# Performance work log

Measured on AMD Instinct MI355X. Metric: run time of the kernel, lower is better.

The kernel has to match this reference:

```python
import jax, jax.numpy as jnp
import numpy as np

N_NODES = 10000
N_EDGES = 160000
N_GRAPHS = 64
D_IN = 128
D_H = 512
N_CLS = 2
L = 3
EPS = 1e-7   # GENConv message eps / clamp min
MAXV = 10.0  # GENConv power-mean clamp max
BN_EPS = 1e-5


def setup_inputs() -> dict:
    key = jax.random.key(0)
    ks = jax.random.split(key, 8)
    return {
        "x": jax.random.normal(ks[0], (N_NODES, D_IN), jnp.float32),
        "W0": jax.random.normal(ks[1], (D_IN, D_H), jnp.float32) * 0.05,
        "Wrest": jax.random.normal(ks[2], (L - 1, D_H, D_H), jnp.float32) * 0.05,
        "bconv": jnp.zeros((L, D_H), jnp.float32),
        "p": jnp.ones((L,), jnp.float32),
        "msg_scale": jnp.ones((L,), jnp.float32),
        "bn_gamma": jnp.ones((L, D_H), jnp.float32),
        "bn_beta": jnp.zeros((L, D_H), jnp.float32),
        "fc1_W": jax.random.normal(ks[3], (2 * D_H, D_H), jnp.float32) * 0.05,
        "fc1_b": jnp.zeros((D_H,), jnp.float32),
        "bn4_g": jnp.ones((D_H,), jnp.float32),
        "bn4_b": jnp.zeros((D_H,), jnp.float32),
        "fc2_W": jax.random.normal(ks[4], (D_H, N_CLS), jnp.float32) * 0.05,
        "fc2_b": jnp.zeros((N_CLS,), jnp.float32),
        "edge_index": jax.random.randint(ks[5], (2, N_EDGES), 0, N_NODES, dtype=jnp.int32),
        "batch": jnp.sort(jax.random.randint(ks[6], (N_NODES,), 0, N_GRAPHS, dtype=jnp.int32)),
    }


def _batchnorm(h, g, b):
    # training-mode BatchNorm1d: batch statistics, biased variance
    mu = h.mean(axis=0)
    var = ((h - mu) ** 2).mean(axis=0)
    return (h - mu) * jax.lax.rsqrt(var + BN_EPS) * g + b


def _genconv(x, W, b, p, scale, src, dst):
    # message: m_e = relu(x_src) + eps  (no edge_attr), clamped to [eps, 10]
    m = jnp.minimum(jax.nn.relu(x[src]) + EPS, MAXV)          # [E, d]
    # power-mean aggregation onto target nodes
    deg = jax.ops.segment_sum(jnp.ones((src.shape[0],), x.dtype), dst, N_NODES)
    agg = jax.ops.segment_sum(m ** p, dst, N_NODES) / jnp.maximum(deg, 1.0)[:, None]
    agg = jnp.clip(agg, EPS, MAXV) ** (1.0 / p)               # [N, d]
    # MessageNorm: l2-normalize aggregated message, rescale by ||x|| * scale
    msg = agg / jnp.maximum(jnp.linalg.norm(agg, axis=-1, keepdims=True), 1e-12)
    xn = jnp.linalg.norm(x, axis=-1, keepdims=True)
    out = x + msg * xn * scale                                # residual add
    return out @ W + b                                        # 1-layer MLP


def reference(x, W0, Wrest, bconv, p, msg_scale, bn_gamma, bn_beta,
              fc1_W, fc1_b, bn4_g, bn4_b, fc2_W, fc2_b, edge_index, batch):
    src, dst = edge_index[0], edge_index[1]
    h = x
    jk = None
    for i in range(L):
        W = W0 if i == 0 else Wrest[i - 1]
        h = _genconv(h, W, bconv[i], p[i], msg_scale[i], src, dst)
        h = jax.nn.relu(_batchnorm(h, bn_gamma[i], bn_beta[i]))
        jk = h if jk is None else jnp.maximum(jk, h)          # JumpingKnowledge 'max'
    # global max + mean pooling per graph
    cnt = jax.ops.segment_sum(jnp.ones((N_NODES,), h.dtype), batch, N_GRAPHS)
    gmean = jax.ops.segment_sum(jk, batch, N_GRAPHS) / jnp.maximum(cnt, 1.0)[:, None]
    gmax = jax.ops.segment_max(jk, batch, N_GRAPHS)
    gmax = jnp.where(cnt[:, None] > 0, gmax, 0.0)
    g = jnp.concatenate([gmax, gmean], axis=1)                # [G, 1024]
    g = jax.nn.relu(_batchnorm(g @ fc1_W + fc1_b, bn4_g, bn4_b))
    # dropout: eval mode (identity)
    return g @ fc2_W + fc2_b                                  # [G, num_classes]
```

## Files before the change

kernel.cpp:

```cpp
#include <hip/hip_runtime.h>
#include <hip/hip_bf16.h>
#include <math.h>

#define N_NODES 10000
#define N_GRAPHS 64
#define N_EDGES 160000
#define D_INPUT 128
#define D_H 512
#define EPS 1e-7f
#define MAXV 10.0f
#define BN_EPS 1e-5f
#define M_PAD 10112

typedef __attribute__((ext_vector_type(4))) float f32x4;
typedef __attribute__((ext_vector_type(8))) __bf16 bf16x8;

__global__ __launch_bounds__(256) void hist_kernel(const int* __restrict__ dst,
                                                   int* __restrict__ cnt) {
  int i = blockIdx.x * blockDim.x + threadIdx.x;
  if (i < N_EDGES) atomicAdd(&cnt[dst[i]], 1);
}

__global__ __launch_bounds__(256) void scan_kernel(int* __restrict__ cnt,
                                                   int* __restrict__ rowptr) {
  __shared__ int ps[256];
  int tid = threadIdx.x;
  const int CH = 40;
  int b0 = tid * CH;
  bool active = (b0 < N_NODES);
  int v[CH];
  int s = 0;
  if (active) {
    const int4* c4p = (const int4*)(cnt + b0);
#pragma unroll
    for (int i = 0; i < CH / 4; i++) {
      int4 q = c4p[i];
      v[4 * i] = q.x; v[4 * i + 1] = q.y; v[4 * i + 2] = q.z; v[4 * i + 3] = q.w;
      s += q.x + q.y + q.z + q.w;
    }
  }
  ps[tid] = s;
  __syncthreads();
  for (int off = 1; off < 256; off <<= 1) {
    int t = (tid >= off) ? ps[tid - off] : 0;
    __syncthreads();
    ps[tid] += t;
    __syncthreads();
  }
  int run = (tid == 0) ? 0 : ps[tid - 1];
  if (active) {
    int r[CH];
#pragma unroll
    for (int i = 0; i < CH; i++) { r[i] = run; run += v[i]; }
    int4* rp = (int4*)(rowptr + b0);
    int4* cz = (int4*)(cnt + b0);
#pragma unroll
    for (int i = 0; i < CH / 4; i++) {
      rp[i] = make_int4(r[4 * i], r[4 * i + 1], r[4 * i + 2], r[4 * i + 3]);
      cz[i] = make_int4(0, 0, 0, 0);
    }
  }
  if (tid == 255) rowptr[N_NODES] = ps[255];
}

__global__ __launch_bounds__(256) void scatter_kernel(
    const int* __restrict__ src, const int* __restrict__ dst,
    const int* __restrict__ rowptr, int* __restrict__ cursor,
    int* __restrict__ csr_src) {
  int i = blockIdx.x * blockDim.x + threadIdx.x;
  if (i < N_EDGES) {
    int t = dst[i];
    int pos = rowptr[t] + atomicAdd(&cursor[t], 1);
    csr_src[pos] = src[i];
  }
}

__global__ __launch_bounds__(512) void bn_affine(float* __restrict__ stats,
                                                 const float* __restrict__ gamma,
                                                 const float* __restrict__ beta,
                                                 float* __restrict__ aff) {
  int c = threadIdx.x;
  const float invN = 1.0f / (float)N_NODES;
  float mean = stats[c] * invN;
  float var = stats[D_H + c] * invN - mean * mean;
  float sc = rsqrtf(var + BN_EPS) * gamma[c];
  aff[c] = sc;
  aff[D_H + c] = beta[c] - mean * sc;
  stats[c] = 0.f;
  stats[D_H + c] = 0.f;
}

__global__ __launch_bounds__(256) void msg0_kernel(const float* __restrict__ x,
                                                   const float* __restrict__ p_ptr,
                                                   __hip_bfloat16* __restrict__ msgb) {
  float p = *p_ptr;
  bool p1 = (p == 1.0f);
  const int total = N_NODES * D_INPUT / 2;
  for (int i = blockIdx.x * 256 + threadIdx.x; i < total; i += gridDim.x * 256) {
    float2 v = ((const float2*)x)[i];
    float m0 = fminf(fmaxf(v.x, 0.f) + EPS, MAXV);
    float m1 = fminf(fmaxf(v.y, 0.f) + EPS, MAXV);
    if (!p1) { m0 = powf(m0, p); m1 = powf(m1, p); }
    __hip_bfloat162 o;
    o.x = __float2bfloat16(m0);
    o.y = __float2bfloat16(m1);
    ((__hip_bfloat162*)msgb)[i] = o;
  }
}

template <int D, bool BN>
__global__ __launch_bounds__(256) void agg_msgnorm_kernel(
    const float* __restrict__ h, const float* __restrict__ aff,
    const __hip_bfloat16* __restrict__ msgb,
    const int* __restrict__ rowptr, const int* __restrict__ csr_src,
    const float* __restrict__ p_ptr, const float* __restrict__ scale_ptr,
    __hip_bfloat16* __restrict__ out) {
  constexpr int C = D / 2;
  constexpr int SL = 256 / C;
  int n = blockIdx.x;
  int tid = threadIdx.x;
  int col = tid % C;
  int slice = tid / C;
  int lo = rowptr[n], hi = rowptr[n + 1];
  float p = *p_ptr;
  float scale = *scale_ptr;
  bool p1 = (p == 1.0f);
  float invp = 1.0f / p;
  float inv_dg = 1.0f / fmaxf((float)(hi - lo), 1.0f);
  const float2* h2 = (const float2*)h;
  const uint* mg = (const uint*)msgb;

  __shared__ int s_src[256];
  float accx = 0.f, accy = 0.f;
  for (int base = lo; base < hi; base += 256) {
    int m = min(256, hi - base);
    __syncthreads();
    if (tid < m) s_src[tid] = csr_src[base + tid];
    __syncthreads();
    int j = slice;
    for (; j + 3 * SL < m; j += 4 * SL) {
      uint u0 = mg[(size_t)s_src[j] * C + col];
      uint u1 = mg[(size_t)s_src[j + SL] * C + col];
      uint u2 = mg[(size_t)s_src[j + 2 * SL] * C + col];
      uint u3 = mg[(size_t)s_src[j + 3 * SL] * C + col];
      accx += (__uint_as_float(u0 << 16) + __uint_as_float(u1 << 16)) +
              (__uint_as_float(u2 << 16) + __uint_as_float(u3 << 16));
      accy += (__uint_as_float(u0 & 0xFFFF0000u) + __uint_as_float(u1 & 0xFFFF0000u)) +
              (__uint_as_float(u2 & 0xFFFF0000u) + __uint_as_float(u3 & 0xFFFF0000u));
    }
    for (; j < m; j += SL) {
      uint u = mg[(size_t)s_src[j] * C + col];
      accx += __uint_as_float(u << 16);
      accy += __uint_as_float(u & 0xFFFF0000u);
    }
  }

  if constexpr (SL > 1) {
    __shared__ float sacc[2][256];
    sacc[0][tid] = accx;
    sacc[1][tid] = accy;
    __syncthreads();
    if (tid < C) {
#pragma unroll
      for (int s = 1; s < SL; s++) {
        accx += sacc[0][s * C + tid];
        accy += sacc[1][s * C + tid];
      }
    }
  }

  float a0 = 0.f, a1 = 0.f, hv0 = 0.f, hv1 = 0.f, sa = 0.f, sh = 0.f;
  if (tid < C) {
    a0 = fminf(fmaxf(accx * inv_dg, EPS), MAXV);
    a1 = fminf(fmaxf(accy * inv_dg, EPS), MAXV);
    if (!p1) { a0 = powf(a0, invp); a1 = powf(a1, invp); }
    float2 hx = h2[(size_t)n * C + tid];
    if constexpr (BN) {
      float2 s2 = ((const float2*)aff)[tid];
      float2 b2 = ((const float2*)(aff + D_H))[tid];
      hx.x = fmaxf(hx.x * s2.x + b2.x, 0.f);
      hx.y = fmaxf(hx.y * s2.y + b2.y, 0.f);
    }
    hv0 = hx.x;
    hv1 = hx.y;
    sa = a0 * a0 + a1 * a1;
    sh = hv0 * hv0 + hv1 * hv1;
  }
  for (int off = 32; off; off >>= 1) {
    sa += __shfl_down(sa, off);
    sh += __shfl_down(sh, off);
  }
  __shared__ float red[2][4];
  __shared__ float tot[2];
  int wid = tid >> 6;
  if ((tid & 63) == 0) { red[0][wid] = sa; red[1][wid] = sh; }
  __syncthreads();
  if (tid == 0) {
    tot[0] = red[0][0] + red[0][1] + red[0][2] + red[0][3];
    tot[1] = red[1][0] + red[1][1] + red[1][2] + red[1][3];
  }
  __syncthreads();
  float k = sqrtf(tot[1]) * scale / fmaxf(sqrtf(tot[0]), 1e-12f);
  if (tid < C) {
    __hip_bfloat162 o2;
    o2.x = __float2bfloat16(hv0 + a0 * k);
    o2.y = __float2bfloat16(hv1 + a1 * k);
    ((__hip_bfloat162*)out)[(size_t)n * C + tid] = o2;
  }
}

__global__ __launch_bounds__(256) void convert_all(
    const float* __restrict__ W0, const float* __restrict__ Wrest,
    __hip_bfloat16* __restrict__ w0t, __hip_bfloat16* __restrict__ w1t,
    __hip_bfloat16* __restrict__ w2t, int* __restrict__ cnt,
    float* __restrict__ stats) {
  int z = blockIdx.z;
  const float* W;
  __hip_bfloat16* Wt;
  int K;
  if (z == 0) { W = W0; Wt = w0t; K = D_INPUT; }
  else if (z == 1) { W = Wrest; Wt = w1t; K = D_H; }
  else { W = Wrest + (size_t)D_H * D_H; Wt = w2t; K = D_H; }

  if (z == 0 && blockIdx.x >= 4) {
    int bid = (blockIdx.x - 4) * 16 + blockIdx.y;
    int idx = bid * 256 + threadIdx.x;
    if (idx < N_NODES) cnt[idx] = 0;
    int sidx = idx - N_NODES;
    if (sidx >= 0 && sidx < 1024) stats[sidx] = 0.f;
    return;
  }

  __shared__ float tile[32][33];
  int k0 = blockIdx.x * 32, n0 = blockIdx.y * 32;
  int tx = threadIdx.x & 31, ty = threadIdx.x >> 5;
  for (int i = ty; i < 32; i += 8)
    tile[i][tx] = W[(size_t)(k0 + i) * D_H + n0 + tx];
  __syncthreads();
  for (int i = ty; i < 32; i += 8)
    Wt[(size_t)(n0 + i) * K + k0 + tx] = __float2bfloat16(tile[tx][i]);
}

__global__ __launch_bounds__(256) void mfma_gemm(
    const __hip_bfloat16* __restrict__ A, const __hip_bfloat16* __restrict__ Bt,
    const float* __restrict__ bias, float* __restrict__ C, float* __restrict__ stats,
    int M, int K) {
  __shared__ ushort As[128 * 64];
  __shared__ ushort Bs[128 * 64];
  __shared__ float sred[128][2];
  int tid = threadIdx.x;
  int l = tid & 63;
  int w = tid >> 6;
  int wm = w >> 1, wn = w & 1;
  int row0 = blockIdx.x * 128;
  int col0 = blockIdx.y * 128;

  f32x4 acc[4][4];
#pragma unroll
  for (int m = 0; m < 4; m++)
#pragma unroll
    for (int n = 0; n < 4; n++) acc[m][n] = (f32x4){0.f, 0.f, 0.f, 0.f};

  const ushort* Ag = (const ushort*)A;
  const ushort* Bg = (const ushort*)Bt;
  char* AsB = (char*)As;
  char* BsB = (char*)Bs;

  if (tid < 128) { sred[tid][0] = 0.f; sred[tid][1] = 0.f; }

  int srow = tid >> 3;
  int scb = (tid & 7) * 16;
  int wbyte = scb ^ ((srow & 7) << 4);
  int scol = scb >> 1;

  int lswz = (l & 7) << 4;
  int kb = (l >> 4) * 16;
  int arow = wm * 64 + (l & 15);
  int brow = wn * 64 + (l & 15);

  for (int k0 = 0; k0 < K; k0 += 64) {
    uint4 ra[4], rb[4];
#pragma unroll
    for (int j = 0; j < 4; j++) {
      int row = j * 32 + srow;
      ra[j] = *(const uint4*)(Ag + (size_t)(row0 + row) * K + k0 + scol);
      rb[j] = *(const uint4*)(Bg + (size_t)(col0 + row) * K + k0 + scol);
    }
#pragma unroll
    for (int j = 0; j < 4; j++) {
      int row = j * 32 + srow;
      *(uint4*)(AsB + row * 128 + wbyte) = ra[j];
      *(uint4*)(BsB + row * 128 + wbyte) = rb[j];
    }
    __syncthreads();
#pragma unroll
    for (int kk = 0; kk < 2; kk++) {
      bf16x8 af[4], bfr[4];
#pragma unroll
      for (int m = 0; m < 4; m++)
        af[m] = *(const bf16x8*)(AsB + (arow + m * 16) * 128 + ((kk * 64 + kb) ^ lswz));
#pragma unroll
      for (int n = 0; n < 4; n++)
        bfr[n] = *(const bf16x8*)(BsB + (brow + n * 16) * 128 + ((kk * 64 + kb) ^ lswz));
#pragma unroll
      for (int m = 0; m < 4; m++)
#pragma unroll
        for (int n = 0; n < 4; n++)
          acc[m][n] = __builtin_amdgcn_mfma_f32_16x16x32_bf16(af[m], bfr[n], acc[m][n], 0, 0, 0);
    }
    __syncthreads();
  }

  int crow0 = row0 + wm * 64 + (l >> 4) * 4;
  int ccol0 = col0 + wn * 64 + (l & 15);
#pragma unroll
  for (int n = 0; n < 4; n++) {
    int col = ccol0 + n * 16;
    float bv = bias[col];
    float ps = 0.f, pq = 0.f;
#pragma unroll
    for (int m = 0; m < 4; m++) {
#pragma unroll
      for (int r = 0; r < 4; r++) {
        int rr = crow0 + m * 16 + r;
        if (rr < M) {
          float v = acc[m][n][r] + bv;
          C[(size_t)rr * D_H + col] = v;
          ps += v;
          pq += v * v;
        }
      }
    }
    ps += __shfl_down(ps, 16); pq += __shfl_down(pq, 16);
    ps += __shfl_down(ps, 32); pq += __shfl_down(pq, 32);
    if ((l >> 4) == 0) {
      atomicAdd(&sred[wn * 64 + n * 16 + (l & 15)][0], ps);
      atomicAdd(&sred[wn * 64 + n * 16 + (l & 15)][1], pq);
    }
  }
  __syncthreads();
  if (tid < 128) {
    atomicAdd(&stats[col0 + tid], sred[tid][0]);
    atomicAdd(&stats[D_H + col0 + tid], sred[tid][1]);
  }
}

template <bool WRITE_MSG>
__global__ __launch_bounds__(256) void jk_msg_update(
    const float* __restrict__ hlin, const float* __restrict__ aff,
    float* __restrict__ jk, const float* __restrict__ p_ptr,
    __hip_bfloat16* __restrict__ msgb, int layer) {
  float p = 1.f;
  bool p1 = true;
  if constexpr (WRITE_MSG) {
    p = *p_ptr;
    p1 = (p == 1.0f);
  }
  const int total = N_NODES * D_H / 4;
  for (int idx = blockIdx.x * blockDim.x + threadIdx.x; idx < total;
       idx += gridDim.x * blockDim.x) {
    int c4 = idx & 127;
    float4 x = ((const float4*)hlin)[idx];
    float4 sc = ((const float4*)aff)[c4];
    float4 sh = ((const float4*)(aff + D_H))[c4];
    float4 v;
    v.x = fmaxf(x.x * sc.x + sh.x, 0.f);
    v.y = fmaxf(x.y * sc.y + sh.y, 0.f);
    v.z = fmaxf(x.z * sc.z + sh.z, 0.f);
    v.w = fmaxf(x.w * sc.w + sh.w, 0.f);
    if constexpr (WRITE_MSG) {
      float m0 = fminf(v.x + EPS, MAXV);
      float m1 = fminf(v.y + EPS, MAXV);
      float m2 = fminf(v.z + EPS, MAXV);
      float m3 = fminf(v.w + EPS, MAXV);
      if (!p1) { m0 = powf(m0, p); m1 = powf(m1, p); m2 = powf(m2, p); m3 = powf(m3, p); }
      __hip_bfloat162 o01, o23;
      o01.x = __float2bfloat16(m0); o01.y = __float2bfloat16(m1);
      o23.x = __float2bfloat16(m2); o23.y = __float2bfloat16(m3);
      ((__hip_bfloat162*)msgb)[2 * idx] = o01;
      ((__hip_bfloat162*)msgb)[2 * idx + 1] = o23;
    }
    if (layer != 0) {
      float4 j = ((const float4*)jk)[idx];
      v.x = fmaxf(v.x, j.x);
      v.y = fmaxf(v.y, j.y);
      v.z = fmaxf(v.z, j.z);
      v.w = fmaxf(v.w, j.w);
    }
    ((float4*)jk)[idx] = v;
  }
}

__device__ __forceinline__ int lower_bound_i(const int* a, int n, int v) {
  int lo = 0, hi = n;
  while (lo < hi) {
    int mid = (lo + hi) >> 1;
    if (a[mid] < v) lo = mid + 1; else hi = mid;
  }
  return lo;
}

__global__ __launch_bounds__(256) void pool_kernel(const float* __restrict__ jk,
                                                   const int* __restrict__ batch,
                                                   float* __restrict__ g) {
  int gid = blockIdx.x;
  int cl = threadIdx.x & 15;
  int slice = threadIdx.x >> 4;
  int f4c = blockIdx.y * 16 + cl;
  int lo = lower_bound_i(batch, N_NODES, gid);
  int hi = lower_bound_i(batch, N_NODES, gid + 1);
  const float4* J = (const float4*)jk;
  float4 mx = make_float4(0.f, 0.f, 0.f, 0.f);
  float4 sm = make_float4(0.f, 0.f, 0.f, 0.f);
  int r = lo + slice;
  for (; r + 16 < hi; r += 32) {
    float4 v0 = J[(size_t)r * 128 + f4c];
    float4 v1 = J[(size_t)(r + 16) * 128 + f4c];
    mx.x = fmaxf(fmaxf(mx.x, v0.x), v1.x);
    mx.y = fmaxf(fmaxf(mx.y, v0.y), v1.y);
    mx.z = fmaxf(fmaxf(mx.z, v0.z), v1.z);
    mx.w = fmaxf(fmaxf(mx.w, v0.w), v1.w);
    sm.x += v0.x + v1.x; sm.y += v0.y + v1.y;
    sm.z += v0.z + v1.z; sm.w += v0.w + v1.w;
  }
  for (; r < hi; r += 16) {
    float4 v = J[(size_t)r * 128 + f4c];
    mx.x = fmaxf(mx.x, v.x); mx.y = fmaxf(mx.y, v.y);
    mx.z = fmaxf(mx.z, v.z); mx.w = fmaxf(mx.w, v.w);
    sm.x += v.x; sm.y += v.y; sm.z += v.z; sm.w += v.w;
  }
  __shared__ float4 smax[16][16];
  __shared__ float4 ssum[16][16];
  smax[slice][cl] = mx;
  ssum[slice][cl] = sm;
  __syncthreads();
  if (slice == 0) {
#pragma unroll
    for (int s = 1; s < 16; s++) {
      float4 m2 = smax[s][cl], s2 = ssum[s][cl];
      mx.x = fmaxf(mx.x, m2.x); mx.y = fmaxf(mx.y, m2.y);
      mx.z = fmaxf(mx.z, m2.z); mx.w = fmaxf(mx.w, m2.w);
      sm.x += s2.x; sm.y += s2.y; sm.z += s2.z; sm.w += s2.w;
    }
    float ic = 1.0f / fmaxf((float)(hi - lo), 1.0f);
    if (hi <= lo) mx = make_float4(0.f, 0.f, 0.f, 0.f);
    sm.x *= ic; sm.y *= ic; sm.z *= ic; sm.w *= ic;
    ((float4*)(g + (size_t)gid * 1024))[f4c] = mx;
    ((float4*)(g + (size_t)gid * 1024 + D_H))[f4c] = sm;
  }
}

__global__ __launch_bounds__(256) void fc1_kernel(const float* __restrict__ g,
                                                  const float* __restrict__ W,
                                                  const float* __restrict__ b,
                                                  float* __restrict__ out) {
  __shared__ float sg[1024];
  __shared__ float sred[4][64];
  int gid = blockIdx.x;
  int tid = threadIdx.x;
  ((float4*)sg)[tid] = ((const float4*)(g + (size_t)gid * 1024))[tid];
  __syncthreads();
  int cl = tid & 63;
  int slice = tid >> 6;
  int col = blockIdx.y * 64 + cl;
  int k0 = slice * 256;
  float acc = 0.f;
#pragma unroll 4
  for (int k = k0; k < k0 + 256; k++) acc += sg[k] * W[(size_t)k * D_H + col];
  sred[slice][cl] = acc;
  __syncthreads();
  if (slice == 0)
    out[(size_t)gid * D_H + col] =
        sred[0][cl] + sred[1][cl] + sred[2][cl] + sred[3][cl] + b[col];
}

__global__ __launch_bounds__(256) void bn4_kernel(const float* __restrict__ x,
                                                  const float* __restrict__ gmm,
                                                  const float* __restrict__ bb,
                                                  float* __restrict__ y) {
  int cl = threadIdx.x & 63;
  int slice = threadIdx.x >> 6;
  int c = blockIdx.x * 64 + cl;
  float s = 0.f, q = 0.f;
#pragma unroll
  for (int r = slice * 16; r < slice * 16 + 16; r++) {
    float v = x[(size_t)r * D_H + c];
    s += v; q += v * v;
  }
  __shared__ float ss[4][64], sq[4][64];
  ss[slice][cl] = s;
  sq[slice][cl] = q;
  __syncthreads();
  float S = ss[0][cl] + ss[1][cl] + ss[2][cl] + ss[3][cl];
  float Q = sq[0][cl] + sq[1][cl] + sq[2][cl] + sq[3][cl];
  float mean = S * (1.0f / N_GRAPHS);
  float var = Q * (1.0f / N_GRAPHS) - mean * mean;
  float rs = rsqrtf(var + BN_EPS) * gmm[c];
  float sh = bb[c] - mean * rs;
#pragma unroll
  for (int r = slice * 16; r < slice * 16 + 16; r++)
    y[(size_t)r * D_H + c] = fmaxf(x[(size_t)r * D_H + c] * rs + sh, 0.f);
}

__global__ __launch_bounds__(64) void fc2_kernel(const float* __restrict__ y,
                                                 const float* __restrict__ W,
                                                 const float* __restrict__ b,
                                                 float* __restrict__ out) {
  int gid = blockIdx.x;
  int lane = threadIdx.x;
  float a0 = 0.f, a1 = 0.f;
  for (int k = lane; k < D_H; k += 64) {
    float v = y[(size_t)gid * D_H + k];
    a0 += v * W[k * 2 + 0];
    a1 += v * W[k * 2 + 1];
  }
  for (int off = 32; off; off >>= 1) {
    a0 += __shfl_down(a0, off);
    a1 += __shfl_down(a1, off);
  }
  if (lane == 0) {
    out[gid * 2 + 0] = a0 + b[0];
    out[gid * 2 + 1] = a1 + b[1];
  }
}

extern "C" void kernel_launch(void* const* d_in, const int* in_sizes, int n_in,
                              void* d_out, int out_size, void* d_ws, size_t ws_size,
                              hipStream_t stream) {
  const float* x       = (const float*)d_in[0];
  const float* W0      = (const float*)d_in[1];
  const float* Wrest   = (const float*)d_in[2];
  const float* bconv   = (const float*)d_in[3];
  const float* p       = (const float*)d_in[4];
  const float* mscale  = (const float*)d_in[5];
  const float* bn_g    = (const float*)d_in[6];
  const float* bn_b    = (const float*)d_in[7];
  const float* fc1_W   = (const float*)d_in[8];
  const float* fc1_b   = (const float*)d_in[9];
  const float* bn4_g   = (const float*)d_in[10];
  const float* bn4_b   = (const float*)d_in[11];
  const float* fc2_W   = (const float*)d_in[12];
  const float* fc2_b   = (const float*)d_in[13];
  const int*   eidx    = (const int*)d_in[14];
  const int*   batch   = (const int*)d_in[15];
  float* out = (float*)d_out;

  const int* src = eidx;
  const int* dst = eidx + N_EDGES;

  float* ws = (float*)d_ws;
  const size_t NH = (size_t)N_NODES * D_H;
  float* hlin  = ws;
  float* jk    = hlin + NH;
  float* stats = jk + NH;
  float* aff   = stats + 1024;
  __hip_bfloat16* residb = (__hip_bfloat16*)(aff + 1024);
  __hip_bfloat16* msgb = residb + (size_t)M_PAD * D_H;
  __hip_bfloat16* w0t = msgb + NH;
  __hip_bfloat16* w1t = w0t + 512 * 128;
  __hip_bfloat16* w2t = w1t + 512 * 512;
  int* cnt     = (int*)(w2t + 512 * 512);
  int* rowptr  = cnt + N_NODES;
  int* csr_src = rowptr + N_NODES + 1;
  float* g     = (float*)(csr_src + N_EDGES);
  float* g2lin = g + 64 * 1024;
  float* g2    = g2lin + 64 * D_H;

  convert_all<<<dim3(16, 16, 3), 256, 0, stream>>>(W0, Wrest, w0t, w1t, w2t, cnt, stats);

  hist_kernel<<<(N_EDGES + 255) / 256, 256, 0, stream>>>(dst, cnt);
  scan_kernel<<<1, 256, 0, stream>>>(cnt, rowptr);
  scatter_kernel<<<(N_EDGES + 255) / 256, 256, 0, stream>>>(src, dst, rowptr, cnt, csr_src);

  msg0_kernel<<<1280, 256, 0, stream>>>(x, p, msgb);

  for (int layer = 0; layer < 3; layer++) {
    if (layer == 0)
      agg_msgnorm_kernel<D_INPUT, false><<<N_NODES, 256, 0, stream>>>(
          x, nullptr, msgb, rowptr, csr_src, p + layer, mscale + layer, residb);
    else
      agg_msgnorm_kernel<D_H, true><<<N_NODES, 256, 0, stream>>>(
          hlin, aff, msgb, rowptr, csr_src, p + layer, mscale + layer, residb);
    const __hip_bfloat16* Wt = (layer == 0) ? w0t : (layer == 1 ? w1t : w2t);
    int K = (layer == 0) ? D_INPUT : D_H;
    mfma_gemm<<<dim3(M_PAD / 128, D_H / 128), 256, 0, stream>>>(
        residb, Wt, bconv + (size_t)layer * D_H, hlin, stats, N_NODES, K);
    bn_affine<<<1, 512, 0, stream>>>(stats, bn_g + (size_t)layer * D_H,
                                     bn_b + (size_t)layer * D_H, aff);
    if (layer < 2)
      jk_msg_update<true><<<2048, 256, 0, stream>>>(hlin, aff, jk, p + layer + 1, msgb, layer);
    else
      jk_msg_update<false><<<2048, 256, 0, stream>>>(hlin, aff, jk, nullptr, nullptr, layer);
  }

  pool_kernel<<<dim3(N_GRAPHS, 8), 256, 0, stream>>>(jk, batch, g);
  fc1_kernel<<<dim3(N_GRAPHS, 8), 256, 0, stream>>>(g, fc1_W, fc1_b, g2lin);
  bn4_kernel<<<8, 256, 0, stream>>>(g2lin, bn4_g, bn4_b, g2);
  fc2_kernel<<<N_GRAPHS, 64, 0, stream>>>(g2, fc2_W, fc2_b, out);
}
```

Measured before the change: 255.9 us.

## Fuse small kernels: hist+msg0, inline BN affine, fuse last JK with pooling, fold BN4

Merges the histogram and first-message kernels into one launch. Removes the separate bn_affine launches by recomputing the BatchNorm scale and shift per element inside jk_msg_update, using per-layer stats buffers. Fuses the final layer's BN/ReLU/JK-max with global max/mean pooling through shared and global atomics, and folds the BN4 statistics into fc1 (atomics) and its application into fc2. Together these cut about seven launches and one full pass over the jk tensor, at the cost of float atomics (nondeterministic sum order) and redundant per-element BN math.

```diff
diff --git a/kernel.cpp b/kernel.cpp
--- a/kernel.cpp
+++ b/kernel.cpp
@@ -15,10 +15,30 @@
 typedef __attribute__((ext_vector_type(4))) float f32x4;
 typedef __attribute__((ext_vector_type(8))) __bf16 bf16x8;
 
-__global__ __launch_bounds__(256) void hist_kernel(const int* __restrict__ dst,
-                                                   int* __restrict__ cnt) {
-  int i = blockIdx.x * blockDim.x + threadIdx.x;
-  if (i < N_EDGES) atomicAdd(&cnt[dst[i]], 1);
+__global__ __launch_bounds__(256) void hist_msg0(const int* __restrict__ dst,
+                                                 int* __restrict__ cnt,
+                                                 const float* __restrict__ x,
+                                                 const float* __restrict__ p_ptr,
+                                                 __hip_bfloat16* __restrict__ msgb) {
+  int bid = blockIdx.x;
+  int tid = threadIdx.x;
+  if (bid < 625) {
+    atomicAdd(&cnt[dst[bid * 256 + tid]], 1);
+    return;
+  }
+  float p = *p_ptr;
+  bool p1 = (p == 1.0f);
+  const int total = N_NODES * D_INPUT / 2;
+  for (int i = (bid - 625) * 256 + tid; i < total; i += 320000) {
+    float2 v = ((const float2*)x)[i];
+    float m0 = fminf(fmaxf(v.x, 0.f) + EPS, MAXV);
+    float m1 = fminf(fmaxf(v.y, 0.f) + EPS, MAXV);
+    if (!p1) { m0 = powf(m0, p); m1 = powf(m1, p); }
+    __hip_bfloat162 o;
+    o.x = __float2bfloat16(m0);
+    o.y = __float2bfloat16(m1);
+    ((__hip_bfloat162*)msgb)[i] = o;
+  }
 }
 
 __global__ __launch_bounds__(256) void scan_kernel(int* __restrict__ cnt,
@@ -72,39 +92,6 @@
     int t = dst[i];
     int pos = rowptr[t] + atomicAdd(&cursor[t], 1);
     csr_src[pos] = src[i];
-  }
-}
-
-__global__ __launch_bounds__(512) void bn_affine(float* __restrict__ stats,
-                                                 const float* __restrict__ gamma,
-                                                 const float* __restrict__ beta,
-                                                 float* __restrict__ aff) {
-  int c = threadIdx.x;
-  const float invN = 1.0f / (float)N_NODES;
-  float mean = stats[c] * invN;
-  float var = stats[D_H + c] * invN - mean * mean;
-  float sc = rsqrtf(var + BN_EPS) * gamma[c];
-  aff[c] = sc;
-  aff[D_H + c] = beta[c] - mean * sc;
-  stats[c] = 0.f;
-  stats[D_H + c] = 0.f;
-}
-
-__global__ __launch_bounds__(256) void msg0_kernel(const float* __restrict__ x,
-                                                   const float* __restrict__ p_ptr,
-                                                   __hip_bfloat16* __restrict__ msgb) {
-  float p = *p_ptr;
-  bool p1 = (p == 1.0f);
-  const int total = N_NODES * D_INPUT / 2;
-  for (int i = blockIdx.x * 256 + threadIdx.x; i < total; i += gridDim.x * 256) {
-    float2 v = ((const float2*)x)[i];
-    float m0 = fminf(fmaxf(v.x, 0.f) + EPS, MAXV);
-    float m1 = fminf(fmaxf(v.y, 0.f) + EPS, MAXV);
-    if (!p1) { m0 = powf(m0, p); m1 = powf(m1, p); }
-    __hip_bfloat162 o;
-    o.x = __float2bfloat16(m0);
-    o.y = __float2bfloat16(m1);
-    ((__hip_bfloat162*)msgb)[i] = o;
   }
 }
 
@@ -213,7 +200,8 @@
     const float* __restrict__ W0, const float* __restrict__ Wrest,
     __hip_bfloat16* __restrict__ w0t, __hip_bfloat16* __restrict__ w1t,
     __hip_bfloat16* __restrict__ w2t, int* __restrict__ cnt,
-    float* __restrict__ stats) {
+    float* __restrict__ stats, float* __restrict__ stats4,
+    float* __restrict__ g) {
   int z = blockIdx.z;
   const float* W;
   __hip_bfloat16* Wt;
@@ -223,11 +211,17 @@
   else { W = Wrest + (size_t)D_H * D_H; Wt = w2t; K = D_H; }
 
   if (z == 0 && blockIdx.x >= 4) {
-    int bid = (blockIdx.x - 4) * 16 + blockIdx.y;
-    int idx = bid * 256 + threadIdx.x;
-    if (idx < N_NODES) cnt[idx] = 0;
-    int sidx = idx - N_NODES;
-    if (sidx >= 0 && sidx < 1024) stats[sidx] = 0.f;
+    int base = ((blockIdx.x - 4) * 16 + blockIdx.y) * 256 + threadIdx.x;
+    const int TOT = 10000 + 3072 + 1024 + 65536;
+    for (int e = base; e < TOT; e += 49152) {
+      if (e < 10000) cnt[e] = 0;
+      else {
+        int f = e - 10000;
+        if (f < 3072) stats[f] = 0.f;
+        else if (f < 4096) stats4[f - 3072] = 0.f;
+        else g[f - 4096] = 0.f;
+      }
+    }
     return;
   }
 
@@ -345,30 +339,45 @@
   }
 }
 
-template <bool WRITE_MSG>
 __global__ __launch_bounds__(256) void jk_msg_update(
-    const float* __restrict__ hlin, const float* __restrict__ aff,
+    const float* __restrict__ hlin, const float* __restrict__ stats,
+    const float* __restrict__ gamma, const float* __restrict__ beta,
     float* __restrict__ jk, const float* __restrict__ p_ptr,
-    __hip_bfloat16* __restrict__ msgb, int layer) {
-  float p = 1.f;
-  bool p1 = true;
-  if constexpr (WRITE_MSG) {
-    p = *p_ptr;
-    p1 = (p == 1.0f);
-  }
+    __hip_bfloat16* __restrict__ msgb, float* __restrict__ aff, int layer) {
+  float p = *p_ptr;
+  bool p1 = (p == 1.0f);
+  const float invN = 1.0f / (float)N_NODES;
   const int total = N_NODES * D_H / 4;
   for (int idx = blockIdx.x * blockDim.x + threadIdx.x; idx < total;
        idx += gridDim.x * blockDim.x) {
     int c4 = idx & 127;
+    float4 s4 = ((const float4*)stats)[c4];
+    float4 q4 = ((const float4*)(stats + D_H))[c4];
+    float4 g4 = ((const float4*)gamma)[c4];
+    float4 b4 = ((const float4*)beta)[c4];
+    float4 sc, sh;
+    {
+      float m0 = s4.x * invN, m1 = s4.y * invN, m2 = s4.z * invN, m3 = s4.w * invN;
+      sc.x = rsqrtf(q4.x * invN - m0 * m0 + BN_EPS) * g4.x;
+      sc.y = rsqrtf(q4.y * invN - m1 * m1 + BN_EPS) * g4.y;
+      sc.z = rsqrtf(q4.z * invN - m2 * m2 + BN_EPS) * g4.z;
+      sc.w = rsqrtf(q4.w * invN - m3 * m3 + BN_EPS) * g4.w;
+      sh.x = b4.x - m0 * sc.x;
+      sh.y = b4.y - m1 * sc.y;
+      sh.z = b4.z - m2 * sc.z;
+      sh.w = b4.w - m3 * sc.w;
+    }
+    if (idx < 128) {
+      ((float4*)aff)[idx] = sc;
+      ((float4*)(aff + D_H))[idx] = sh;
+    }
     float4 x = ((const float4*)hlin)[idx];
-    float4 sc = ((const float4*)aff)[c4];
-    float4 sh = ((const float4*)(aff + D_H))[c4];
     float4 v;
     v.x = fmaxf(x.x * sc.x + sh.x, 0.f);
     v.y = fmaxf(x.y * sc.y + sh.y, 0.f);
     v.z = fmaxf(x.z * sc.z + sh.z, 0.f);
     v.w = fmaxf(x.w * sc.w + sh.w, 0.f);
-    if constexpr (WRITE_MSG) {
+    {
       float m0 = fminf(v.x + EPS, MAXV);
       float m1 = fminf(v.y + EPS, MAXV);
       float m2 = fminf(v.z + EPS, MAXV);
@@ -391,6 +400,121 @@
   }
 }
 
+__global__ __launch_bounds__(256) void jk_pool_kernel(
+    const float* __restrict__ hlin, const float* __restrict__ stats,
+    const float* __restrict__ gamma, const float* __restrict__ beta,
+    const float* __restrict__ jk, const int* __restrict__ batch,
+    float* __restrict__ g) {
+  int tid = threadIdx.x;
+  int f4l = tid & 31;
+  int rs = tid >> 5;
+  int row0 = blockIdx.x * 128;
+  int c4 = blockIdx.y * 32 + f4l;
+
+  __shared__ int s_batch[128];
+  __shared__ int lmax[4][32][4];
+  __shared__ float lsum[4][32][4];
+  if (tid < 128) {
+    int r = row0 + tid;
+    s_batch[tid] = (r < N_NODES) ? batch[r] : -1;
+  }
+  for (int i = tid; i < 512; i += 256) {
+    ((int*)lmax)[i] = 0;
+    ((float*)lsum)[i] = 0.f;
+  }
+  __syncthreads();
+  int g_first = s_batch[0];
+
+  const float invN = 1.0f / (float)N_NODES;
+  float4 s4 = ((const float4*)stats)[c4];
+  float4 q4 = ((const float4*)(stats + D_H))[c4];
+  float4 g4 = ((const float4*)gamma)[c4];
+  float4 b4 = ((const float4*)beta)[c4];
+  float4 sc, sh;
+  {
+    float m0 = s4.x * invN, m1 = s4.y * invN, m2 = s4.z * invN, m3 = s4.w * invN;
+    sc.x = rsqrtf(q4.x * invN - m0 * m0 + BN_EPS) * g4.x;
+    sc.y = rsqrtf(q4.y * invN - m1 * m1 + BN_EPS) * g4.y;
+    sc.z = rsqrtf(q4.z * invN - m2 * m2 + BN_EPS) * g4.z;
+    sc.w = rsqrtf(q4.w * invN - m3 * m3 + BN_EPS) * g4.w;
+    sh.x = b4.x - m0 * sc.x;
+    sh.y = b4.y - m1 * sc.y;
+    sh.z = b4.z - m2 * sc.z;
+    sh.w = b4.w - m3 * sc.w;
+  }
+
+  float4 mx = make_float4(0.f, 0.f, 0.f, 0.f);
+  float4 sm = make_float4(0.f, 0.f, 0.f, 0.f);
+  int cur = -1;
+
+#define FLUSH()                                                              \
+  do {                                                                       \
+    int slot = cur - g_first;                                                \
+    if (slot < 4) {                                                          \
+      atomicMax(&lmax[slot][f4l][0], __float_as_int(mx.x));                  \
+      atomicMax(&lmax[slot][f4l][1], __float_as_int(mx.y));                  \
+      atomicMax(&lmax[slot][f4l][2], __float_as_int(mx.z));                  \
+      atomicMax(&lmax[slot][f4l][3], __float_as_int(mx.w));                  \
+      atomicAdd(&lsum[slot][f4l][0], sm.x);                                  \
+      atomicAdd(&lsum[slot][f4l][1], sm.y);                                  \
+      atomicAdd(&lsum[slot][f4l][2], sm.z);                                  \
+      atomicAdd(&lsum[slot][f4l][3], sm.w);                                  \
+    } else {                                                                 \
+      int cb = c4 * 4;                                                       \
+      atomicMax((int*)&g[(size_t)cur * 1024 + cb + 0], __float_as_int(mx.x)); \
+      atomicMax((int*)&g[(size_t)cur * 1024 + cb + 1], __float_as_int(mx.y)); \
+      atomicMax((int*)&g[(size_t)cur * 1024 + cb + 2], __float_as_int(mx.z)); \
+      atomicMax((int*)&g[(size_t)cur * 1024 + cb + 3], __float_as_int(mx.w)); \
+      atomicAdd(&g[(size_t)cur * 1024 + 512 + cb + 0], sm.x);                \
+      atomicAdd(&g[(size_t)cur * 1024 + 512 + cb + 1], sm.y);                \
+      atomicAdd(&g[(size_t)cur * 1024 + 512 + cb + 2], sm.z);                \
+      atomicAdd(&g[(size_t)cur * 1024 + 512 + cb + 3], sm.w);                \
+    }                                                                        \
+  } while (0)
+
+  for (int i = 0; i < 16; i++) {
+    int r = row0 + rs + i * 8;
+    if (r >= N_NODES) break;
+    int gg = s_batch[rs + i * 8];
+    if (gg != cur) {
+      if (cur >= 0) FLUSH();
+      cur = gg;
+      mx = make_float4(0.f, 0.f, 0.f, 0.f);
+      sm = make_float4(0.f, 0.f, 0.f, 0.f);
+    }
+    float4 x = ((const float4*)hlin)[(size_t)r * 128 + c4];
+    float4 j4 = ((const float4*)jk)[(size_t)r * 128 + c4];
+    float4 v;
+    v.x = fmaxf(fmaxf(x.x * sc.x + sh.x, 0.f), j4.x);
+    v.y = fmaxf(fmaxf(x.y * sc.y + sh.y, 0.f), j4.y);
+    v.z = fmaxf(fmaxf(x.z * sc.z + sh.z, 0.f), j4.z);
+    v.w = fmaxf(fmaxf(x.w * sc.w + sh.w, 0.f), j4.w);
+    mx.x = fmaxf(mx.x, v.x); mx.y = fmaxf(mx.y, v.y);
+    mx.z = fmaxf(mx.z, v.z); mx.w = fmaxf(mx.w, v.w);
+    sm.x += v.x; sm.y += v.y; sm.z += v.z; sm.w += v.w;
+  }
+  if (cur >= 0) FLUSH();
+#undef FLUSH
+  __syncthreads();
+
+  int last = min(127, N_NODES - 1 - row0);
+  int g_last = s_batch[last];
+  int ns = min(3, g_last - g_first);
+  for (int s = 0; s <= ns; s++) {
+    int gi = g_first + s;
+    if (tid < 128) {
+      int fc = tid >> 2, comp = tid & 3;
+      int col = (blockIdx.y * 32 + fc) * 4 + comp;
+      atomicMax((int*)&g[(size_t)gi * 1024 + col], lmax[s][fc][comp]);
+    } else {
+      int t = tid - 128;
+      int fc = t >> 2, comp = t & 3;
+      int col = (blockIdx.y * 32 + fc) * 4 + comp;
+      atomicAdd(&g[(size_t)gi * 1024 + 512 + col], lsum[s][fc][comp]);
+    }
+  }
+}
+
 __device__ __forceinline__ int lower_bound_i(const int* a, int n, int v) {
   int lo = 0, hi = n;
   while (lo < hi) {
@@ -400,65 +524,24 @@
   return lo;
 }
 
-__global__ __launch_bounds__(256) void pool_kernel(const float* __restrict__ jk,
-                                                   const int* __restrict__ batch,
-                                                   float* __restrict__ g) {
-  int gid = blockIdx.x;
-  int cl = threadIdx.x & 15;
-  int slice = threadIdx.x >> 4;
-  int f4c = blockIdx.y * 16 + cl;
-  int lo = lower_bound_i(batch, N_NODES, gid);
-  int hi = lower_bound_i(batch, N_NODES, gid + 1);
-  const float4* J = (const float4*)jk;
-  float4 mx = make_float4(0.f, 0.f, 0.f, 0.f);
-  float4 sm = make_float4(0.f, 0.f, 0.f, 0.f);
-  int r = lo + slice;
-  for (; r + 16 < hi; r += 32) {
-    float4 v0 = J[(size_t)r * 128 + f4c];
-    float4 v1 = J[(size_t)(r + 16) * 128 + f4c];
-    mx.x = fmaxf(fmaxf(mx.x, v0.x), v1.x);
-    mx.y = fmaxf(fmaxf(mx.y, v0.y), v1.y);
-    mx.z = fmaxf(fmaxf(mx.z, v0.z), v1.z);
-    mx.w = fmaxf(fmaxf(mx.w, v0.w), v1.w);
-    sm.x += v0.x + v1.x; sm.y += v0.y + v1.y;
-    sm.z += v0.z + v1.z; sm.w += v0.w + v1.w;
-  }
-  for (; r < hi; r += 16) {
-    float4 v = J[(size_t)r * 128 + f4c];
-    mx.x = fmaxf(mx.x, v.x); mx.y = fmaxf(mx.y, v.y);
-    mx.z = fmaxf(mx.z, v.z); mx.w = fmaxf(mx.w, v.w);
-    sm.x += v.x; sm.y += v.y; sm.z += v.z; sm.w += v.w;
-  }
-  __shared__ float4 smax[16][16];
-  __shared__ float4 ssum[16][16];
-  smax[slice][cl] = mx;
-  ssum[slice][cl] = sm;
-  __syncthreads();
-  if (slice == 0) {
-#pragma unroll
-    for (int s = 1; s < 16; s++) {
-      float4 m2 = smax[s][cl], s2 = ssum[s][cl];
-      mx.x = fmaxf(mx.x, m2.x); mx.y = fmaxf(mx.y, m2.y);
-      mx.z = fmaxf(mx.z, m2.z); mx.w = fmaxf(mx.w, m2.w);
-      sm.x += s2.x; sm.y += s2.y; sm.z += s2.z; sm.w += s2.w;
-    }
-    float ic = 1.0f / fmaxf((float)(hi - lo), 1.0f);
-    if (hi <= lo) mx = make_float4(0.f, 0.f, 0.f, 0.f);
-    sm.x *= ic; sm.y *= ic; sm.z *= ic; sm.w *= ic;
-    ((float4*)(g + (size_t)gid * 1024))[f4c] = mx;
-    ((float4*)(g + (size_t)gid * 1024 + D_H))[f4c] = sm;
-  }
-}
-
 __global__ __launch_bounds__(256) void fc1_kernel(const float* __restrict__ g,
+                                                  const int* __restrict__ batch,
                                                   const float* __restrict__ W,
                                                   const float* __restrict__ b,
-                                                  float* __restrict__ out) {
+                                                  float* __restrict__ out,
+                                                  float* __restrict__ stats4) {
   __shared__ float sg[1024];
   __shared__ float sred[4][64];
   int gid = blockIdx.x;
   int tid = threadIdx.x;
-  ((float4*)sg)[tid] = ((const float4*)(g + (size_t)gid * 1024))[tid];
+  int lo = lower_bound_i(batch, N_NODES, gid);
+  int hi = lower_bound_i(batch, N_NODES, gid + 1);
+  float inv_cnt = 1.0f / fmaxf((float)(hi - lo), 1.0f);
+  float4 gv = ((const float4*)(g + (size_t)gid * 1024))[tid];
+  if (tid >= 128) {
+    gv.x *= inv_cnt; gv.y *= inv_cnt; gv.z *= inv_cnt; gv.w *= inv_cnt;
+  }
+  ((float4*)sg)[tid] = gv;
   __syncthreads();
   int cl = tid & 63;
   int slice = tid >> 6;
@@ -469,48 +552,32 @@
   for (int k = k0; k < k0 + 256; k++) acc += sg[k] * W[(size_t)k * D_H + col];
   sred[slice][cl] = acc;
   __syncthreads();
-  if (slice == 0)
-    out[(size_t)gid * D_H + col] =
-        sred[0][cl] + sred[1][cl] + sred[2][cl] + sred[3][cl] + b[col];
-}
-
-__global__ __launch_bounds__(256) void bn4_kernel(const float* __restrict__ x,
-                                                  const float* __restrict__ gmm,
-                                                  const float* __restrict__ bb,
-                                                  float* __restrict__ y) {
-  int cl = threadIdx.x & 63;
-  int slice = threadIdx.x >> 6;
-  int c = blockIdx.x * 64 + cl;
-  float s = 0.f, q = 0.f;
-#pragma unroll
-  for (int r = slice * 16; r < slice * 16 + 16; r++) {
-    float v = x[(size_t)r * D_H + c];
-    s += v; q += v * v;
-  }
-  __shared__ float ss[4][64], sq[4][64];
-  ss[slice][cl] = s;
-  sq[slice][cl] = q;
-  __syncthreads();
-  float S = ss[0][cl] + ss[1][cl] + ss[2][cl] + ss[3][cl];
-  float Q = sq[0][cl] + sq[1][cl] + sq[2][cl] + sq[3][cl];
-  float mean = S * (1.0f / N_GRAPHS);
-  float var = Q * (1.0f / N_GRAPHS) - mean * mean;
-  float rs = rsqrtf(var + BN_EPS) * gmm[c];
-  float sh = bb[c] - mean * rs;
-#pragma unroll
-  for (int r = slice * 16; r < slice * 16 + 16; r++)
-    y[(size_t)r * D_H + c] = fmaxf(x[(size_t)r * D_H + c] * rs + sh, 0.f);
+  if (slice == 0) {
+    float v = sred[0][cl] + sred[1][cl] + sred[2][cl] + sred[3][cl] + b[col];
+    out[(size_t)gid * D_H + col] = v;
+    atomicAdd(&stats4[col], v);
+    atomicAdd(&stats4[D_H + col], v * v);
+  }
 }
 
 __global__ __launch_bounds__(64) void fc2_kernel(const float* __restrict__ y,
+                                                 const float* __restrict__ stats4,
+                                                 const float* __restrict__ gmm,
+                                                 const float* __restrict__ bb,
                                                  const float* __restrict__ W,
                                                  const float* __restrict__ b,
                                                  float* __restrict__ out) {
   int gid = blockIdx.x;
   int lane = threadIdx.x;
+  const float invG = 1.0f / (float)N_GRAPHS;
   float a0 = 0.f, a1 = 0.f;
-  for (int k = lane; k < D_H; k += 64) {
-    float v = y[(size_t)gid * D_H + k];
+#pragma unroll
+  for (int j = 0; j < 8; j++) {
+    int k = lane + j * 64;
+    float mean = stats4[k] * invG;
+    float var = stats4[D_H + k] * invG - mean * mean;
+    float sc = rsqrtf(var + BN_EPS) * gmm[k];
+    float v = fmaxf(y[(size_t)gid * D_H + k] * sc + bb[k] - mean * sc, 0.f);
     a0 += v * W[k * 2 + 0];
     a1 += v * W[k * 2 + 1];
   }
@@ -550,10 +617,11 @@
 
   float* ws = (float*)d_ws;
   const size_t NH = (size_t)N_NODES * D_H;
-  float* hlin  = ws;
-  float* jk    = hlin + NH;
-  float* stats = jk + NH;
-  float* aff   = stats + 1024;
+  float* hlin   = ws;
+  float* jk     = hlin + NH;
+  float* stats  = jk + NH;
+  float* stats4 = stats + 3072;
+  float* aff    = stats4 + 1024;
   __hip_bfloat16* residb = (__hip_bfloat16*)(aff + 1024);
   __hip_bfloat16* msgb = residb + (size_t)M_PAD * D_H;
   __hip_bfloat16* w0t = msgb + NH;
@@ -564,15 +632,12 @@
   int* csr_src = rowptr + N_NODES + 1;
   float* g     = (float*)(csr_src + N_EDGES);
   float* g2lin = g + 64 * 1024;
-  float* g2    = g2lin + 64 * D_H;
-
-  convert_all<<<dim3(16, 16, 3), 256, 0, stream>>>(W0, Wrest, w0t, w1t, w2t, cnt, stats);
-
-  hist_kernel<<<(N_EDGES + 255) / 256, 256, 0, stream>>>(dst, cnt);
+
+  convert_all<<<dim3(16, 16, 3), 256, 0, stream>>>(W0, Wrest, w0t, w1t, w2t,
+                                                   cnt, stats, stats4, g);
+  hist_msg0<<<1875, 256, 0, stream>>>(dst, cnt, x, p, msgb);
   scan_kernel<<<1, 256, 0, stream>>>(cnt, rowptr);
   scatter_kernel<<<(N_EDGES + 255) / 256, 256, 0, stream>>>(src, dst, rowptr, cnt, csr_src);
-
-  msg0_kernel<<<1280, 256, 0, stream>>>(x, p, msgb);
 
   for (int layer = 0; layer < 3; layer++) {
     if (layer == 0)
@@ -583,18 +648,20 @@
           hlin, aff, msgb, rowptr, csr_src, p + layer, mscale + layer, residb);
     const __hip_bfloat16* Wt = (layer == 0) ? w0t : (layer == 1 ? w1t : w2t);
     int K = (layer == 0) ? D_INPUT : D_H;
+    float* stats_l = stats + layer * 1024;
     mfma_gemm<<<dim3(M_PAD / 128, D_H / 128), 256, 0, stream>>>(
-        residb, Wt, bconv + (size_t)layer * D_H, hlin, stats, N_NODES, K);
-    bn_affine<<<1, 512, 0, stream>>>(stats, bn_g + (size_t)layer * D_H,
-                                     bn_b + (size_t)layer * D_H, aff);
+        residb, Wt, bconv + (size_t)layer * D_H, hlin, stats_l, N_NODES, K);
     if (layer < 2)
-      jk_msg_update<true><<<2048, 256, 0, stream>>>(hlin, aff, jk, p + layer + 1, msgb, layer);
+      jk_msg_update<<<2048, 256, 0, stream>>>(hlin, stats_l, bn_g + (size_t)layer * D_H,
+                                              bn_b + (size_t)layer * D_H, jk,
+                                              p + layer + 1, msgb, aff, layer);
     else
-      jk_msg_update<false><<<2048, 256, 0, stream>>>(hlin, aff, jk, nullptr, nullptr, layer);
-  }
-
-  pool_kernel<<<dim3(N_GRAPHS, 8), 256, 0, stream>>>(jk, batch, g);
-  fc1_kernel<<<dim3(N_GRAPHS, 8), 256, 0, stream>>>(g, fc1_W, fc1_b, g2lin);
-  bn4_kernel<<<8, 256, 0, stream>>>(g2lin, bn4_g, bn4_b, g2);
-  fc2_kernel<<<N_GRAPHS, 64, 0, stream>>>(g2, fc2_W, fc2_b, out);
-}
+      jk_pool_kernel<<<dim3(79, 4), 256, 0, stream>>>(hlin, stats_l,
+                                                      bn_g + (size_t)layer * D_H,
+                                                      bn_b + (size_t)layer * D_H,
+                                                      jk, batch, g);
+  }
+
+  fc1_kernel<<<dim3(N_GRAPHS, 8), 256, 0, stream>>>(g, batch, fc1_W, fc1_b, g2lin, stats4);
+  fc2_kernel<<<N_GRAPHS, 64, 0, stream>>>(g2lin, stats4, bn4_g, bn4_b, fc2_W, fc2_b, out);
+}
```

After: 243.9 us. 4.7% less time.
